# Kernel tuning notes

Hardware: AMD Instinct MI355X
Metric: run time of the kernel (lower is better)

## Reference

```python
import jax, jax.numpy as jnp
import numpy as np

HEADS, LEVELS, POINTS, DIMS = 8, 4, 4, 256
CH = DIMS // HEADS
SHAPES = np.array([[96, 96], [48, 48], [24, 24], [12, 12]], dtype=np.int64)
LEVEL_START = np.concatenate([[0], np.cumsum(SHAPES[:, 0] * SHAPES[:, 1])[:-1]]).astype(np.int64)
HW = int((SHAPES[:, 0] * SHAPES[:, 1]).sum())
N, Q = 2, HW


def setup_inputs() -> dict:
    key = jax.random.key(0)
    ks = jax.random.split(key, 8)
    return {
        "q": jax.random.normal(ks[0], (N, Q, DIMS), jnp.float32),
        "p": jax.random.uniform(ks[1], (N, Q, LEVELS, 2), jnp.float32),
        "v": jax.random.normal(ks[2], (N, HW, DIMS), jnp.float32),
        "W_off": jax.random.normal(ks[3], (DIMS, HEADS * LEVELS * POINTS * 2), jnp.float32) * 0.01,
        "b_off": jax.random.normal(ks[4], (HEADS * LEVELS * POINTS * 2,), jnp.float32) * 0.5,
        "W_attn": jax.random.normal(ks[5], (DIMS, HEADS * LEVELS * POINTS), jnp.float32) * 0.02,
        "b_attn": jnp.zeros((HEADS * LEVELS * POINTS,), jnp.float32),
        "W_in": jax.random.normal(ks[6], (DIMS, DIMS), jnp.float32) / np.float32(np.sqrt(DIMS)),
        "b_in": jnp.zeros((DIMS,), jnp.float32),
        "W_out": jax.random.normal(ks[7], (DIMS, DIMS), jnp.float32) / np.float32(np.sqrt(DIMS)),
        "b_out": jnp.zeros((DIMS,), jnp.float32),
        "shapes": jnp.asarray(SHAPES),
        "level_index": jnp.asarray(LEVEL_START),
    }


def _sample_level(vl, loc_l, Hl, Wl):
    """Bilinear sample with zero padding outside the feature map.
    vl: [N, Hl*Wl, heads, C]; loc_l: [N, Q, heads, P, 2] normalized (x, y) in [0,1].
    Returns [N, Q, P, heads, C]."""
    Nb, Qn, Hd, P, _ = loc_l.shape
    x = loc_l[..., 0] * Wl - 0.5  # pixel coords, align_corners=False convention
    y = loc_l[..., 1] * Hl - 0.5
    x0 = jnp.floor(x)
    y0 = jnp.floor(y)
    dx = x - x0
    dy = y - y0
    x0i = x0.astype(jnp.int32)
    y0i = y0.astype(jnp.int32)
    out = jnp.zeros((Nb, Qn, P, Hd, vl.shape[-1]), vl.dtype)
    corners = ((x0i, y0i, (1 - dx) * (1 - dy)), (x0i + 1, y0i, dx * (1 - dy)),
               (x0i, y0i + 1, (1 - dx) * dy), (x0i + 1, y0i + 1, dx * dy))
    for cx, cy, w in corners:
        valid = (cx >= 0) & (cx < Wl) & (cy >= 0) & (cy < Hl)
        idx = jnp.clip(cy, 0, Hl - 1) * Wl + jnp.clip(cx, 0, Wl - 1)  # [N,Q,Hd,P]
        idx_t = idx.transpose(0, 1, 3, 2).reshape(Nb, Qn * P, Hd, 1)
        g = jnp.take_along_axis(vl, idx_t, axis=1).reshape(Nb, Qn, P, Hd, -1)
        wv = jnp.where(valid, w, 0.0).transpose(0, 1, 3, 2)  # [N,Q,P,Hd]
        out = out + g * wv[..., None].astype(vl.dtype)
    return out


def _forward(q, p, v, W_off, b_off, W_attn, b_attn, W_in, b_in, W_out, b_out, shp, lsi):
    Nb, Qn, _ = q.shape
    v = (v @ W_in + b_in).reshape(Nb, -1, HEADS, CH)
    off = (q @ W_off + b_off).reshape(Nb, Qn, HEADS, LEVELS, POINTS, 2)
    attn = jax.nn.softmax((q @ W_attn + b_attn).reshape(Nb, Qn, HEADS, LEVELS * POINTS), axis=-1)
    attn = attn.reshape(Nb, Qn, HEADS, LEVELS, POINTS)
    # offsets normalized by (W, H) of each level, added to reference points (2-coord branch)
    off_norm = jnp.asarray(np.stack([shp[:, 1], shp[:, 0]], -1), q.dtype)  # [L, 2]
    loc = p[:, :, None, :, None, :] + off / off_norm[None, None, None, :, None, :]  # [N,Q,Hd,L,P,2]
    out = jnp.zeros((Nb, Qn, HEADS, CH), q.dtype)
    for l in range(LEVELS):
        Hl, Wl = int(shp[l, 0]), int(shp[l, 1])
        s = int(lsi[l])
        vl = jax.lax.slice_in_dim(v, s, s + Hl * Wl, axis=1)
        samp = _sample_level(vl, loc[:, :, :, l], Hl, Wl)  # [N,Q,P,Hd,C]
        out = out + jnp.einsum('nqphc,nqhp->nqhc', samp, attn[:, :, :, l])
    return out.reshape(Nb, Qn, DIMS) @ W_out + b_out


def reference(q, p, v, W_off, b_off, W_attn, b_attn, W_in, b_in, W_out, b_out, shapes, level_index):
    shp = np.asarray(shapes)  # spatial shapes are structural constants
    lsi = np.asarray(level_index)
    return _forward(q, p, v, W_off, b_off, W_attn, b_attn, W_in, b_in, W_out, b_out, shp, lsi)
```

## Files before the change

### kernel.cpp

```cpp
#include <hip/hip_runtime.h>
#include <hip/hip_bf16.h>
#include <math.h>

#define NB      2
#define QN      12240
#define HW_TOT  12240
#define DIMS    256
#define HEADS   8
#define CH      32
#define LEVELS  4
#define POINTS  4
#define M_TOT   (NB * QN)

typedef unsigned short ushort_t;
typedef __attribute__((ext_vector_type(8))) short short8;
typedef __attribute__((ext_vector_type(4))) float floatx4;

__device__ __forceinline__ ushort_t f2bf(float f) {
    __hip_bfloat16 h = __float2bfloat16(f);
    return *reinterpret_cast<ushort_t*>(&h);
}

__global__ __launch_bounds__(256) void convert_qv_kernel(
    const float* __restrict__ v, const float* __restrict__ q,
    ushort_t* __restrict__ vbf, ushort_t* __restrict__ qbf)
{
    const size_t i = ((size_t)blockIdx.x * 256 + threadIdx.x) * 8;
    const size_t half = (size_t)M_TOT * DIMS;
    const float* src; ushort_t* dst; size_t off;
    if (i < half) { src = v; dst = vbf; off = i; }
    else          { src = q; dst = qbf; off = i - half; }
    const float4 a = *(const float4*)&src[off];
    const float4 b = *(const float4*)&src[off + 4];
    ushort_t t[8] = {f2bf(a.x), f2bf(a.y), f2bf(a.z), f2bf(a.w),
                     f2bf(b.x), f2bf(b.y), f2bf(b.z), f2bf(b.w)};
    *(int4*)&dst[off] = *(int4*)t;
}

__global__ __launch_bounds__(256) void prep_weights_kernel(
    const float* __restrict__ W_in, const float* __restrict__ W_off,
    const float* __restrict__ W_attn, const float* __restrict__ W_out,
    const float* __restrict__ b_off, const float* __restrict__ b_attn,
    ushort_t* __restrict__ Tin, ushort_t* __restrict__ Tcomb,
    ushort_t* __restrict__ Tout, float* __restrict__ bcomb)
{
    const int z  = blockIdx.z;
    const int gi = blockIdx.x * 256 + threadIdx.x;
    if (z == 1 && gi < 384)
        bcomb[gi] = (gi < 256) ? b_off[gi] : b_attn[gi - 256];
    const int Nw = (z == 1) ? 384 : 256;
    if (gi >= Nw * 256) return;
    const int k = gi & 255;
    const int n = gi >> 8;
    float val; ushort_t* T;
    if (z == 0)      { val = W_in[k * 256 + n];  T = Tin;  }
    else if (z == 1) { val = (n < 256) ? W_off[k * 256 + n]
                                       : W_attn[k * 128 + (n - 256)]; T = Tcomb; }
    else             { val = W_out[k * 256 + n]; T = Tout; }
    T[n * 256 + k] = f2bf(val);
}

__device__ __forceinline__ void gemm_tile_core(
    const ushort_t* __restrict__ A, const ushort_t* __restrict__ BT,
    const float* __restrict__ bias, void* __restrict__ C, bool c_bf16,
    int M, int Nc, int bm0, int bn0, int K,
    ushort_t* As, ushort_t* Bs)
{
    const int tid  = threadIdx.x;
    const int wave = tid >> 6;
    const int lane = tid & 63;
    const int quad = lane >> 4;
    const int l16  = lane & 15;
    const int wm   = (wave >> 1) * 64;
    const int wn   = (wave & 1) * 64;

    const int off0 = tid * 16;
    const int row0 = off0 >> 6;
    const int kc0  = (off0 & 63) >> 1;

    int ar0 = bm0 + row0;      if (ar0 > M - 1) ar0 = M - 1;
    int ar1 = bm0 + row0 + 64; if (ar1 > M - 1) ar1 = M - 1;

    const ushort_t* ga0 = A  + (size_t)ar0 * K + kc0;
    const ushort_t* ga1 = A  + (size_t)ar1 * K + kc0;
    const ushort_t* gb0 = BT + (size_t)(bn0 + row0) * K + kc0;
    const ushort_t* gb1 = BT + (size_t)(bn0 + row0 + 64) * K + kc0;

    ushort_t* lA0 = As + wave * 512;
    ushort_t* lA1 = As + wave * 512 + 2048;
    ushort_t* lB0 = Bs + wave * 512;
    ushort_t* lB1 = Bs + wave * 512 + 2048;

    floatx4 acc[4][4];
    #pragma unroll
    for (int i = 0; i < 4; ++i)
        #pragma unroll
        for (int j = 0; j < 4; ++j)
            acc[i][j] = (floatx4){0.f, 0.f, 0.f, 0.f};

    for (int kk = 0; kk < K; kk += 32) {
        __builtin_amdgcn_global_load_lds(
            (const __attribute__((address_space(1))) void*)(ga0 + kk),
            (__attribute__((address_space(3))) void*)lA0, 16, 0, 0);
        __builtin_amdgcn_global_load_lds(
            (const __attribute__((address_space(1))) void*)(ga1 + kk),
            (__attribute__((address_space(3))) void*)lA1, 16, 0, 0);
        __builtin_amdgcn_global_load_lds(
            (const __attribute__((address_space(1))) void*)(gb0 + kk),
            (__attribute__((address_space(3))) void*)lB0, 16, 0, 0);
        __builtin_amdgcn_global_load_lds(
            (const __attribute__((address_space(1))) void*)(gb1 + kk),
            (__attribute__((address_space(3))) void*)lB1, 16, 0, 0);
        __syncthreads();

        short8 af[4], bfr[4];
        #pragma unroll
        for (int mt = 0; mt < 4; ++mt)
            af[mt] = *(const short8*)&As[(wm + mt * 16 + l16) * 32 + quad * 8];
        #pragma unroll
        for (int nt = 0; nt < 4; ++nt)
            bfr[nt] = *(const short8*)&Bs[(wn + nt * 16 + l16) * 32 + quad * 8];
        #pragma unroll
        for (int mt = 0; mt < 4; ++mt)
            #pragma unroll
            for (int nt = 0; nt < 4; ++nt)
                acc[mt][nt] = __builtin_amdgcn_mfma_f32_16x16x32_bf16(
                    af[mt], bfr[nt], acc[mt][nt], 0, 0, 0);
        __syncthreads();
    }

    #pragma unroll
    for (int mt = 0; mt < 4; ++mt) {
        #pragma unroll
        for (int j = 0; j < 4; ++j) {
            const int row = bm0 + wm + mt * 16 + quad * 4 + j;
            if (row >= M) continue;
            #pragma unroll
            for (int nt = 0; nt < 4; ++nt) {
                const int col = bn0 + wn + nt * 16 + l16;
                const float val = acc[mt][nt][j] + bias[col];
                if (c_bf16) ((ushort_t*)C)[(size_t)row * Nc + col] = f2bf(val);
                else        ((float*)C)[(size_t)row * Nc + col]    = val;
            }
        }
    }
}

__global__ __launch_bounds__(256) void gemm_proj_kernel(
    const ushort_t* __restrict__ vbf, const ushort_t* __restrict__ qbf,
    const ushort_t* __restrict__ Tin, const ushort_t* __restrict__ Tcomb,
    const float* __restrict__ b_in, const float* __restrict__ bcomb,
    ushort_t* __restrict__ vproj, float* __restrict__ offlog)
{
    __shared__ ushort_t As[128 * 32];
    __shared__ ushort_t Bs[128 * 32];
    const int bm0 = blockIdx.x * 128;
    const int y = blockIdx.y;
    if (y < 2)
        gemm_tile_core(vbf, Tin, b_in, vproj, true, M_TOT, 256, bm0, y * 128, 256, As, Bs);
    else
        gemm_tile_core(qbf, Tcomb, bcomb, offlog, false, M_TOT, 384, bm0, (y - 2) * 128, 256, As, Bs);
}

__global__ __launch_bounds__(256) void gemm_out_kernel(
    const ushort_t* __restrict__ mid, const ushort_t* __restrict__ Tout,
    const float* __restrict__ b_out, float* __restrict__ out)
{
    __shared__ ushort_t As[128 * 32];
    __shared__ ushort_t Bs[128 * 32];
    gemm_tile_core(mid, Tout, b_out, out, false, M_TOT, 256,
                   blockIdx.x * 128, blockIdx.y * 128, 256, As, Bs);
}

#define ACC4(W, g) \
    ax = fmaf(W, __uint_as_float(g.x << 16), ax);          \
    ay = fmaf(W, __uint_as_float(g.x & 0xffff0000u), ay);  \
    az = fmaf(W, __uint_as_float(g.y << 16), az);          \
    aw = fmaf(W, __uint_as_float(g.y & 0xffff0000u), aw);

__global__ __launch_bounds__(256, 8) void msda_sample_kernel(
    const ushort_t* __restrict__ vproj, const float* __restrict__ offlog,
    const float* __restrict__ p, ushort_t* __restrict__ mid)
{
    __shared__ int s_buf[4096];

    const int tid = threadIdx.x;
    const int wv  = tid >> 6;
    const int l   = tid & 63;
    const int nq  = blockIdx.x * 4 + wv;
    const int nb  = (nq >= QN) ? 1 : 0;

    const size_t orow = (size_t)nq * 384;
    const float2 off0 = *(const float2*)&offlog[orow + 2 * l];
    const float2 off1 = *(const float2*)&offlog[orow + 128 + 2 * l];
    const float  lg0  = offlog[orow + 256 + l];
    const float  lg1  = offlog[orow + 320 + l];
    const int    lvl  = (l >> 2) & 3;
    const float2 pl   = *(const float2*)&p[(size_t)nq * 8 + lvl * 2];

    float m0 = lg0, m1 = lg1;
    #pragma unroll
    for (int m = 8; m; m >>= 1) {
        m0 = fmaxf(m0, __shfl_xor(m0, m));
        m1 = fmaxf(m1, __shfl_xor(m1, m));
    }
    const float e0 = __expf(lg0 - m0);
    const float e1 = __expf(lg1 - m1);
    float s0 = e0, s1 = e1;
    #pragma unroll
    for (int m = 8; m; m >>= 1) {
        s0 += __shfl_xor(s0, m);
        s1 += __shfl_xor(s1, m);
    }
    const float wt0 = e0 * __builtin_amdgcn_rcpf(s0);
    const float wt1 = e1 * __builtin_amdgcn_rcpf(s1);

    const int   Wl    = 96 >> lvl;
    const float fW    = (float)Wl;
    const int   st    = 12288 - (12288 >> (2 * lvl));
    const int   h4    = l >> 4;
    const int   baseb = nb * (HW_TOT * 512) + st * 512;
    const int   sw    = h4 << 3;
    const int   wbase = wv * 1024 + l * 8;

    #pragma unroll
    for (int set = 0; set < 2; ++set) {
        const float ox = set ? off1.x : off0.x;
        const float oy = set ? off1.y : off0.y;
        const float wt = set ? wt1 : wt0;
        const int   h  = set ? (h4 + 4) : h4;

        const float x  = fmaf(pl.x, fW, ox) - 0.5f;
        const float y  = fmaf(pl.y, fW, oy) - 0.5f;
        const float xf = floorf(x), yf = floorf(y);
        const float dx = x - xf,    dy = y - yf;
        const int   x0 = (int)xf,   y0 = (int)yf;
        const bool vx0 = (unsigned)x0       < (unsigned)Wl;
        const bool vx1 = (unsigned)(x0 + 1) < (unsigned)Wl;
        const bool vy0 = (unsigned)y0       < (unsigned)Wl;
        const bool vy1 = (unsigned)(y0 + 1) < (unsigned)Wl;

        const int b00 = baseb + (y0 * Wl + x0) * 512 + h * 64;
        const int b01 = b00 + 512;
        const int b10 = b00 + (Wl << 9);
        const int b11 = b10 + 512;

        const float wy0f = wt * (1.0f - dy), wy1f = wt * dy;
        const float w00 = (vx0 && vy0) ? (1.0f - dx) * wy0f : 0.0f;
        const float w01 = (vx1 && vy0) ? dx * wy0f          : 0.0f;
        const float w10 = (vx0 && vy1) ? (1.0f - dx) * wy1f : 0.0f;
        const float w11 = (vx1 && vy1) ? dx * wy1f          : 0.0f;
        const int   i00 = (vx0 && vy0) ? b00 : 0;
        const int   i01 = (vx1 && vy0) ? b01 : 0;
        const int   i10 = (vx0 && vy1) ? b10 : 0;
        const int   i11 = (vx1 && vy1) ? b11 : 0;

        const int o = (wbase + set * 512) ^ sw;
        *(int4*)&s_buf[o]     = (int4){__float_as_int(w00), i00, __float_as_int(w01), i01};
        *(int4*)&s_buf[o + 4] = (int4){__float_as_int(w10), i10, __float_as_int(w11), i11};
    }

    __builtin_amdgcn_wave_barrier();
    asm volatile("s_waitcnt lgkmcnt(0)" ::: "memory");
    __builtin_amdgcn_wave_barrier();

    const int h   = l >> 3;
    const int c4  = l & 7;
    const int rb  = wv * 1024 + (h >> 2) * 512 + (h & 3) * 128;
    const int sw2 = (h & 3) << 3;
    const char* __restrict__ vb = (const char*)vproj;

    float ax = 0.f, ay = 0.f, az = 0.f, aw = 0.f;
    #pragma unroll 2
    for (int t = 0; t < 16; ++t) {
        const int o = rb + ((t * 8) ^ sw2);
        const int4 cA = *(const int4*)&s_buf[o];
        const int4 cB = *(const int4*)&s_buf[o + 4];
        const uint2 g0 = *(const uint2*)(vb + (unsigned)(cA.y + c4 * 8));
        const uint2 g1 = *(const uint2*)(vb + (unsigned)(cA.w + c4 * 8));
        const uint2 g2 = *(const uint2*)(vb + (unsigned)(cB.y + c4 * 8));
        const uint2 g3 = *(const uint2*)(vb + (unsigned)(cB.w + c4 * 8));
        const float W0 = __int_as_float(cA.x), W1 = __int_as_float(cA.z);
        const float W2 = __int_as_float(cB.x), W3 = __int_as_float(cB.z);
        ACC4(W0, g0);
        ACC4(W1, g1);
        ACC4(W2, g2);
        ACC4(W3, g3);
    }

    ushort_t mv[4] = {f2bf(ax), f2bf(ay), f2bf(az), f2bf(aw)};
    *(uint2*)&mid[(size_t)nq * 256 + l * 4] = *(uint2*)mv;
}

extern "C" void kernel_launch(void* const* d_in, const int* in_sizes, int n_in,
                              void* d_out, int out_size, void* d_ws, size_t ws_size,
                              hipStream_t stream)
{
    const float* q      = (const float*)d_in[0];
    const float* p      = (const float*)d_in[1];
    const float* v      = (const float*)d_in[2];
    const float* W_off  = (const float*)d_in[3];
    const float* b_off  = (const float*)d_in[4];
    const float* W_attn = (const float*)d_in[5];
    const float* b_attn = (const float*)d_in[6];
    const float* W_in   = (const float*)d_in[7];
    const float* b_in   = (const float*)d_in[8];
    const float* W_out  = (const float*)d_in[9];
    const float* b_out  = (const float*)d_in[10];
    float* out = (float*)d_out;

    const int M = M_TOT;

    ushort_t* vproj  = (ushort_t*)d_ws;
    float*    offlog = (float*)(vproj + (size_t)M * 256);
    ushort_t* vbf    = (ushort_t*)(offlog + (size_t)M * 384);
    ushort_t* mid    = vbf;
    ushort_t* qbf    = vbf + (size_t)M * 256;
    ushort_t* Tin    = qbf + (size_t)M * 256;
    ushort_t* Tcomb  = Tin + 256 * 256;
    ushort_t* Tout   = Tcomb + 384 * 256;
    float*    bcomb  = (float*)(Tout + 256 * 256);

    convert_qv_kernel<<<dim3(6120), 256, 0, stream>>>(v, q, vbf, qbf);
    prep_weights_kernel<<<dim3(384, 1, 3), 256, 0, stream>>>(
        W_in, W_off, W_attn, W_out, b_off, b_attn, Tin, Tcomb, Tout, bcomb);

    gemm_proj_kernel<<<dim3(192, 5), 256, 0, stream>>>(
        vbf, qbf, Tin, Tcomb, b_in, bcomb, vproj, offlog);
    msda_sample_kernel<<<dim3(M / 4), 256, 0, stream>>>(vproj, offlog, p, mid);
    gemm_out_kernel<<<dim3(192, 2), 256, 0, stream>>>(mid, Tout, b_out, out);
}
```

Baseline: 197.3 us.

## Store value projection head-major and gather adjacent x-corners in one load

The value-projection GEMM now writes its bf16 output in a head-major layout ([head][row][32 ch]), so the two horizontally adjacent bilinear corners are contiguous 64-byte runs. The sampler stores one row base plus left/right weights per y-row and loads 16 bytes per lane covering both x-corners, which halves the number of gather instructions. A lane-pair shuffle then reduces the partial sums. Out-of-range x-corners are handled by clamping and zero weights, and a zeroed pad region after vproj absorbs over-reads. The cost is scattered 2-byte stores in the GEMM epilogue, extra shuffles, and reads of some bytes that get zero weight.

```diff
diff --git a/kernel.cpp b/kernel.cpp
--- a/kernel.cpp
+++ b/kernel.cpp
@@ -42,10 +42,12 @@
     const float* __restrict__ W_attn, const float* __restrict__ W_out,
     const float* __restrict__ b_off, const float* __restrict__ b_attn,
     ushort_t* __restrict__ Tin, ushort_t* __restrict__ Tcomb,
-    ushort_t* __restrict__ Tout, float* __restrict__ bcomb)
+    ushort_t* __restrict__ Tout, float* __restrict__ bcomb,
+    int* __restrict__ vpad)
 {
     const int z  = blockIdx.z;
     const int gi = blockIdx.x * 256 + threadIdx.x;
+    if (z == 0 && gi < 32) vpad[gi] = 0;
     if (z == 1 && gi < 384)
         bcomb[gi] = (gi < 256) ? b_off[gi] : b_attn[gi - 256];
     const int Nw = (z == 1) ? 384 : 256;
@@ -139,8 +141,12 @@
             for (int nt = 0; nt < 4; ++nt) {
                 const int col = bn0 + wn + nt * 16 + l16;
                 const float val = acc[mt][nt][j] + bias[col];
-                if (c_bf16) ((ushort_t*)C)[(size_t)row * Nc + col] = f2bf(val);
-                else        ((float*)C)[(size_t)row * Nc + col]    = val;
+                if (c_bf16) {
+                    const size_t idx = (((size_t)(col >> 5) * M + row) << 5) + (col & 31);
+                    ((ushort_t*)C)[idx] = f2bf(val);
+                } else {
+                    ((float*)C)[(size_t)row * Nc + col] = val;
+                }
             }
         }
     }
@@ -172,11 +178,13 @@
                    blockIdx.x * 128, blockIdx.y * 128, 256, As, Bs);
 }
 
-#define ACC4(W, g) \
-    ax = fmaf(W, __uint_as_float(g.x << 16), ax);          \
-    ay = fmaf(W, __uint_as_float(g.x & 0xffff0000u), ay);  \
-    az = fmaf(W, __uint_as_float(g.y << 16), az);          \
-    aw = fmaf(W, __uint_as_float(g.y & 0xffff0000u), aw);
+#define LO32(u) __uint_as_float((u) << 16)
+#define HI32(u) __uint_as_float((u) & 0xffff0000u)
+#define ACC8(W, g) \
+    a0 = fmaf(W, LO32(g.x), a0);  a1 = fmaf(W, HI32(g.x), a1); \
+    a2 = fmaf(W, LO32(g.y), a2);  a3 = fmaf(W, HI32(g.y), a3); \
+    a4 = fmaf(W, LO32(g.z), a4);  a5 = fmaf(W, HI32(g.z), a5); \
+    a6 = fmaf(W, LO32(g.w), a6);  a7 = fmaf(W, HI32(g.w), a7);
 
 __global__ __launch_bounds__(256, 8) void msda_sample_kernel(
     const ushort_t* __restrict__ vproj, const float* __restrict__ offlog,
@@ -189,6 +197,7 @@
     const int l   = tid & 63;
     const int nq  = blockIdx.x * 4 + wv;
     const int nb  = (nq >= QN) ? 1 : 0;
+    const int wbase = wv * 1024;
 
     const size_t orow = (size_t)nq * 384;
     const float2 off0 = *(const float2*)&offlog[orow + 2 * l];
@@ -215,13 +224,10 @@
     const float wt0 = e0 * __builtin_amdgcn_rcpf(s0);
     const float wt1 = e1 * __builtin_amdgcn_rcpf(s1);
 
-    const int   Wl    = 96 >> lvl;
-    const float fW    = (float)Wl;
-    const int   st    = 12288 - (12288 >> (2 * lvl));
-    const int   h4    = l >> 4;
-    const int   baseb = nb * (HW_TOT * 512) + st * 512;
-    const int   sw    = h4 << 3;
-    const int   wbase = wv * 1024 + l * 8;
+    const int   Wl  = 96 >> lvl;
+    const float fW  = (float)Wl;
+    const int   st  = 12288 - (12288 >> (2 * lvl));
+    const int   h4  = l >> 4;
 
     #pragma unroll
     for (int set = 0; set < 2; ++set) {
@@ -235,61 +241,74 @@
         const float xf = floorf(x), yf = floorf(y);
         const float dx = x - xf,    dy = y - yf;
         const int   x0 = (int)xf,   y0 = (int)yf;
-        const bool vx0 = (unsigned)x0       < (unsigned)Wl;
-        const bool vx1 = (unsigned)(x0 + 1) < (unsigned)Wl;
+        const bool vxl = (unsigned)x0       < (unsigned)Wl;
+        const bool vxr = (unsigned)(x0 + 1) < (unsigned)Wl;
         const bool vy0 = (unsigned)y0       < (unsigned)Wl;
         const bool vy1 = (unsigned)(y0 + 1) < (unsigned)Wl;
 
-        const int b00 = baseb + (y0 * Wl + x0) * 512 + h * 64;
-        const int b01 = b00 + 512;
-        const int b10 = b00 + (Wl << 9);
-        const int b11 = b10 + 512;
+        const float wxl = vxl ? (1.0f - dx) : (vxr ? dx : 0.0f);
+        const float wxr = (vxl && vxr) ? dx : 0.0f;
+        const int   xb  = vxl ? x0 : 0;
 
         const float wy0f = wt * (1.0f - dy), wy1f = wt * dy;
-        const float w00 = (vx0 && vy0) ? (1.0f - dx) * wy0f : 0.0f;
-        const float w01 = (vx1 && vy0) ? dx * wy0f          : 0.0f;
-        const float w10 = (vx0 && vy1) ? (1.0f - dx) * wy1f : 0.0f;
-        const float w11 = (vx1 && vy1) ? dx * wy1f          : 0.0f;
-        const int   i00 = (vx0 && vy0) ? b00 : 0;
-        const int   i01 = (vx1 && vy0) ? b01 : 0;
-        const int   i10 = (vx0 && vy1) ? b10 : 0;
-        const int   i11 = (vx1 && vy1) ? b11 : 0;
-
-        const int o = (wbase + set * 512) ^ sw;
-        *(int4*)&s_buf[o]     = (int4){__float_as_int(w00), i00, __float_as_int(w01), i01};
-        *(int4*)&s_buf[o + 4] = (int4){__float_as_int(w10), i10, __float_as_int(w11), i11};
+        const float w_l0 = vy0 ? wxl * wy0f : 0.0f;
+        const float w_r0 = vy0 ? wxr * wy0f : 0.0f;
+        const float w_l1 = vy1 ? wxl * wy1f : 0.0f;
+        const float w_r1 = vy1 ? wxr * wy1f : 0.0f;
+
+        int yc0 = y0;     if (yc0 < 0) yc0 = 0; if (yc0 > Wl - 1) yc0 = Wl - 1;
+        int yc1 = y0 + 1; if (yc1 < 0) yc1 = 0; if (yc1 > Wl - 1) yc1 = Wl - 1;
+
+        const int rowb = h * M_TOT + nb * HW_TOT + st + xb;
+        const int lin0 = rowb + yc0 * Wl;
+        const int lin1 = rowb + yc1 * Wl;
+
+        const int a  = l * 16 + set * 8;
+        const int ph = (a ^ (((a >> 8) & 3) << 2)) + wbase;
+        *(int4*)&s_buf[ph] = (int4){lin0 << 6, __float_as_int(w_l0),
+                                    __float_as_int(w_r0), lin1 << 6};
+        *(int2*)&s_buf[ph ^ 4] = (int2){__float_as_int(w_l1), __float_as_int(w_r1)};
     }
 
     __builtin_amdgcn_wave_barrier();
     asm volatile("s_waitcnt lgkmcnt(0)" ::: "memory");
     __builtin_amdgcn_wave_barrier();
 
-    const int h   = l >> 3;
-    const int c4  = l & 7;
-    const int rb  = wv * 1024 + (h >> 2) * 512 + (h & 3) * 128;
-    const int sw2 = (h & 3) << 3;
+    const int  h    = l >> 3;
+    const int  c16  = (l & 7) * 16;
+    const bool hicn = (l & 4) != 0;
+    const int  rbas = (h & 3) * 256 + (h >> 2) * 8;
     const char* __restrict__ vb = (const char*)vproj;
 
-    float ax = 0.f, ay = 0.f, az = 0.f, aw = 0.f;
+    float a0 = 0.f, a1 = 0.f, a2 = 0.f, a3 = 0.f;
+    float a4 = 0.f, a5 = 0.f, a6 = 0.f, a7 = 0.f;
+
     #pragma unroll 2
     for (int t = 0; t < 16; ++t) {
-        const int o = rb + ((t * 8) ^ sw2);
-        const int4 cA = *(const int4*)&s_buf[o];
-        const int4 cB = *(const int4*)&s_buf[o + 4];
-        const uint2 g0 = *(const uint2*)(vb + (unsigned)(cA.y + c4 * 8));
-        const uint2 g1 = *(const uint2*)(vb + (unsigned)(cA.w + c4 * 8));
-        const uint2 g2 = *(const uint2*)(vb + (unsigned)(cB.y + c4 * 8));
-        const uint2 g3 = *(const uint2*)(vb + (unsigned)(cB.w + c4 * 8));
-        const float W0 = __int_as_float(cA.x), W1 = __int_as_float(cA.z);
-        const float W2 = __int_as_float(cB.x), W3 = __int_as_float(cB.z);
-        ACC4(W0, g0);
-        ACC4(W1, g1);
-        ACC4(W2, g2);
-        ACC4(W3, g3);
-    }
-
-    ushort_t mv[4] = {f2bf(ax), f2bf(ay), f2bf(az), f2bf(aw)};
-    *(uint2*)&mid[(size_t)nq * 256 + l * 4] = *(uint2*)mv;
+        const int ia = rbas + t * 16;
+        const int ph = (ia ^ (((ia >> 8) & 3) << 2)) + wbase;
+        const int4 cA = *(const int4*)&s_buf[ph];
+        const int2 cB = *(const int2*)&s_buf[ph ^ 4];
+        const uint4 g0 = *(const uint4*)(vb + (unsigned)(cA.x + c16));
+        const uint4 g1 = *(const uint4*)(vb + (unsigned)(cA.w + c16));
+        const float w0 = hicn ? __int_as_float(cA.z) : __int_as_float(cA.y);
+        const float w1 = hicn ? __int_as_float(cB.y) : __int_as_float(cB.x);
+        ACC8(w0, g0);
+        ACC8(w1, g1);
+    }
+
+    a0 += __shfl_xor(a0, 4);  a1 += __shfl_xor(a1, 4);
+    a2 += __shfl_xor(a2, 4);  a3 += __shfl_xor(a3, 4);
+    a4 += __shfl_xor(a4, 4);  a5 += __shfl_xor(a5, 4);
+    a6 += __shfl_xor(a6, 4);  a7 += __shfl_xor(a7, 4);
+
+    const float o0 = hicn ? a4 : a0;
+    const float o1 = hicn ? a5 : a1;
+    const float o2 = hicn ? a6 : a2;
+    const float o3 = hicn ? a7 : a3;
+    ushort_t mv[4] = {f2bf(o0), f2bf(o1), f2bf(o2), f2bf(o3)};
+    const int col = h * 32 + (l & 3) * 8 + (l & 4);
+    *(uint2*)&mid[(size_t)nq * 256 + col] = *(uint2*)mv;
 }
 
 extern "C" void kernel_launch(void* const* d_in, const int* in_sizes, int n_in,
@@ -312,7 +331,8 @@
     const int M = M_TOT;
 
     ushort_t* vproj  = (ushort_t*)d_ws;
-    float*    offlog = (float*)(vproj + (size_t)M * 256);
+    ushort_t* vpad   = vproj + (size_t)M * 256;
+    float*    offlog = (float*)(vpad + 64);
     ushort_t* vbf    = (ushort_t*)(offlog + (size_t)M * 384);
     ushort_t* mid    = vbf;
     ushort_t* qbf    = vbf + (size_t)M * 256;
@@ -323,7 +343,8 @@
 
     convert_qv_kernel<<<dim3(6120), 256, 0, stream>>>(v, q, vbf, qbf);
     prep_weights_kernel<<<dim3(384, 1, 3), 256, 0, stream>>>(
-        W_in, W_off, W_attn, W_out, b_off, b_attn, Tin, Tcomb, Tout, bcomb);
+        W_in, W_off, W_attn, W_out, b_off, b_attn, Tin, Tcomb, Tout, bcomb,
+        (int*)vpad);
 
     gemm_proj_kernel<<<dim3(192, 5), 256, 0, stream>>>(
         vbf, qbf, Tin, Tcomb, b_in, bcomb, vproj, offlog);
```

New measurement: 188.7 us. 1.05x faster.
